# Kernel tuning notes

Measured on AMD Instinct MI355X. Metric: run time of the kernel, lower is better.

## Reference

```python
import jax, jax.numpy as jnp
import numpy as np

NUM_HEADS = 8


def setup_inputs() -> dict:
    key = jax.random.key(0)
    ks = jax.random.split(key, 7)
    R, C, E = 64, 2048, 512
    x = jax.random.normal(ks[0], (R, C, E), dtype=jnp.float32)
    s = 0.02
    Wq = jax.random.normal(ks[1], (E, E), dtype=jnp.float32) * s
    bq = jax.random.normal(ks[2], (E,), dtype=jnp.float32) * s
    Wk = jax.random.normal(ks[3], (E, E), dtype=jnp.float32) * s
    bk = jax.random.normal(ks[4], (E,), dtype=jnp.float32) * s
    Wv = jax.random.normal(ks[5], (E, E), dtype=jnp.float32) * s
    bv = jax.random.normal(ks[6], (E,), dtype=jnp.float32) * s
    return {"x": x, "Wq": Wq, "bq": bq, "Wk": Wk, "bk": bk, "Wv": Wv, "bv": bv}


def reference(x, Wq, bq, Wk, bk, Wv, bv):
    # pred() path (forward default return_attn=True)
    R, C, E = x.shape
    H = NUM_HEADS
    D = E // H
    # projections (torch Linear: x @ W.T + b), split heads -> [R, H, C, D]
    q = (x @ Wq.T + bq).reshape(R, C, H, D).transpose(0, 2, 1, 3)
    k = (x @ Wk.T + bk).reshape(R, C, H, D).transpose(0, 2, 1, 3)
    v = (x @ Wv.T + bv).reshape(R, C, H, D).transpose(0, 2, 1, 3)
    # mean over rows for q, k -> [H, C, D]; v keeps rows -> [R, H, C, D]
    q = q.mean(axis=0)
    k = k.mean(axis=0)
    # kernelized attention: softmax over feature dim for q, over seq dim for k
    q = jax.nn.softmax(q, axis=-1) * (D ** -0.5)
    k = jax.nn.softmax(k, axis=-2)
    # explicit attention map [H, C, C] (pred path materializes it)
    attn_weights = jnp.einsum('hnd,hmd->hnm', q, k)
    # linear-attention: kv outer-sum context then q @ context
    context = jnp.einsum('hnd,bhne->bhde', k, v)        # [R, H, D, D]
    out = jnp.einsum('hnd,bhde->bhne', q, context)      # [R, H, C, D]
    out = out.transpose(0, 2, 1, 3).reshape(R, C, E)
    return out, attn_weights
```

## Files before the change

### kernel.cpp

```cpp
#include <hip/hip_runtime.h>

#define R_ 64
#define C_ 2048
#define E_ 512
#define H_ 8
#define D_ 64

constexpr int CE = C_ * E_;
constexpr long long OUT_ELEMS = 67108864LL;

typedef __attribute__((ext_vector_type(8))) short bf16x8;
typedef __attribute__((ext_vector_type(4))) float f32x4;

__device__ __forceinline__ unsigned short f2bf(float f) {
    union { float f; unsigned u; } v; v.f = f;
    unsigned r = v.u + 0x7FFFu + ((v.u >> 16) & 1u);
    return (unsigned short)(r >> 16);
}

typedef __attribute__((address_space(1))) unsigned char glob_t;
typedef __attribute__((address_space(3))) unsigned char lds_t;
__device__ __forceinline__ void gld_lds16(const unsigned short* g, unsigned short* l) {
    __builtin_amdgcn_global_load_lds((const glob_t*)g, (lds_t*)l, 16, 0, 0);
}

__global__ __launch_bounds__(256) void prep(const float* __restrict__ x,
                                            float* __restrict__ xbar,
                                            unsigned short* __restrict__ xT) {
    __shared__ float Ts[64][65];
    int c0 = blockIdx.x * 64, e0 = blockIdx.y * 64;
    int t = threadIdx.x;
    int r = t >> 2;
    int cs = (t & 3) * 16;
    float acc[16] = {};
    for (int b = 0; b < 64; ++b) {
        const float* xp = x + ((size_t)b * C_ + c0 + r) * E_ + e0 + cs;
        float vv[16];
        float4 v0 = *(const float4*)(xp);
        float4 v1 = *(const float4*)(xp + 4);
        float4 v2 = *(const float4*)(xp + 8);
        float4 v3 = *(const float4*)(xp + 12);
        vv[0]=v0.x; vv[1]=v0.y; vv[2]=v0.z; vv[3]=v0.w;
        vv[4]=v1.x; vv[5]=v1.y; vv[6]=v1.z; vv[7]=v1.w;
        vv[8]=v2.x; vv[9]=v2.y; vv[10]=v2.z; vv[11]=v2.w;
        vv[12]=v3.x; vv[13]=v3.y; vv[14]=v3.z; vv[15]=v3.w;
        #pragma unroll
        for (int i = 0; i < 16; ++i) acc[i] += vv[i];
        __syncthreads();
        #pragma unroll
        for (int i = 0; i < 16; ++i) Ts[cs + i][r] = vv[i];
        __syncthreads();
        unsigned short ob[16];
        #pragma unroll
        for (int i = 0; i < 16; ++i) ob[i] = f2bf(Ts[r][cs + i]);
        unsigned short* op = xT + ((size_t)b * E_ + e0 + r) * C_ + c0 + cs;
        *(bf16x8*)(op)     = *(bf16x8*)(ob);
        *(bf16x8*)(op + 8) = *(bf16x8*)(ob + 8);
    }
    float* xb = xbar + (size_t)(c0 + r) * E_ + e0 + cs;
    #pragma unroll
    for (int i = 0; i < 16; ++i) xb[i] = acc[i] * 0.015625f;
}

__global__ __launch_bounds__(256) void gemm_nt(const float* __restrict__ A, int lda,
                                               const float* __restrict__ B, int ldb,
                                               float* __restrict__ Cmat, int ldc, int K,
                                               const float* __restrict__ bias, int biasPerM) {
    __shared__ float As[64][65];
    __shared__ float Bs[64][65];
    int m0 = blockIdx.y * 64, n0 = blockIdx.x * 64;
    int t = threadIdx.x, tx = t & 15, ty = t >> 4;
    float acc[4][4] = {};
    for (int k0 = 0; k0 < K; k0 += 64) {
        #pragma unroll
        for (int i = 0; i < 4; ++i) {
            int rr = ty + i * 16, cc = tx * 4;
            float4 av = *(const float4*)(A + (size_t)(m0 + rr) * lda + k0 + cc);
            As[rr][cc] = av.x; As[rr][cc + 1] = av.y; As[rr][cc + 2] = av.z; As[rr][cc + 3] = av.w;
            float4 bv = *(const float4*)(B + (size_t)(n0 + rr) * ldb + k0 + cc);
            Bs[cc][rr] = bv.x; Bs[cc + 1][rr] = bv.y; Bs[cc + 2][rr] = bv.z; Bs[cc + 3][rr] = bv.w;
        }
        __syncthreads();
        for (int kk = 0; kk < 64; ++kk) {
            float a[4];
            #pragma unroll
            for (int i = 0; i < 4; ++i) a[i] = As[ty + 16 * i][kk];
            float4 b4 = *(const float4*)(&Bs[kk][tx * 4]);
            #pragma unroll
            for (int i = 0; i < 4; ++i) {
                acc[i][0] += a[i] * b4.x; acc[i][1] += a[i] * b4.y;
                acc[i][2] += a[i] * b4.z; acc[i][3] += a[i] * b4.w;
            }
        }
        __syncthreads();
    }
    #pragma unroll
    for (int i = 0; i < 4; ++i) {
        int m = m0 + ty + 16 * i, n = n0 + tx * 4;
        float4 o;
        if (biasPerM) {
            float bm = bias[m];
            o.x = acc[i][0] + bm; o.y = acc[i][1] + bm; o.z = acc[i][2] + bm; o.w = acc[i][3] + bm;
        } else {
            o.x = acc[i][0] + bias[n]; o.y = acc[i][1] + bias[n + 1];
            o.z = acc[i][2] + bias[n + 2]; o.w = acc[i][3] + bias[n + 3];
        }
        *(float4*)(Cmat + (size_t)m * ldc + n) = o;
    }
}

__global__ __launch_bounds__(256) void softmax_q(float* __restrict__ q) {
    int t = threadIdx.x;
    int chunk = blockIdx.x * 4 + (t >> 6);
    int lane = t & 63;
    float* p = q + (size_t)chunk * 64;
    float v = p[lane];
    float m = v;
    for (int o = 32; o; o >>= 1) m = fmaxf(m, __shfl_xor(m, o));
    float e = expf(v - m);
    float s = e;
    for (int o = 32; o; o >>= 1) s += __shfl_xor(s, o);
    p[lane] = e / s * 0.125f;
}

__global__ __launch_bounds__(256) void softmax_k(float* __restrict__ kT,
                                                 unsigned short* __restrict__ kbf) {
    __shared__ float red[256];
    int j = blockIdx.x, t = threadIdx.x;
    float* row = kT + (size_t)j * C_;
    float vals[8];
    float mx = -1e30f;
    #pragma unroll
    for (int i = 0; i < 8; ++i) { vals[i] = row[t + 256 * i]; mx = fmaxf(mx, vals[i]); }
    red[t] = mx; __syncthreads();
    for (int s = 128; s; s >>= 1) { if (t < s) red[t] = fmaxf(red[t], red[t + s]); __syncthreads(); }
    mx = red[0]; __syncthreads();
    float sum = 0.f;
    #pragma unroll
    for (int i = 0; i < 8; ++i) { vals[i] = expf(vals[i] - mx); sum += vals[i]; }
    red[t] = sum; __syncthreads();
    for (int s = 128; s; s >>= 1) { if (t < s) red[t] += red[t + s]; __syncthreads(); }
    float inv = 1.0f / red[0];
    #pragma unroll
    for (int i = 0; i < 8; ++i) {
        float v = vals[i] * inv;
        row[t + 256 * i] = v;
        kbf[(size_t)j * C_ + t + 256 * i] = f2bf(v);
    }
}

__global__ __launch_bounds__(256) void t_gemm(const unsigned short* __restrict__ Abf,
                                              const unsigned short* __restrict__ xT,
                                              float* __restrict__ Tout) {
    __shared__ __align__(16) unsigned short As[128 * 32];
    __shared__ __align__(16) unsigned short Bs[128 * 32];
    const int b = blockIdx.z;
    const unsigned short* Bg = xT + (size_t)b * CE;
    const int m0 = blockIdx.y * 128, n0 = blockIdx.x * 128;
    const int t = threadIdx.x, lane = t & 63, w = t >> 6;
    const int wm = (w >> 1) * 64, wn = (w & 1) * 64;
    const int l15 = lane & 15, quad = lane >> 4;
    const int srow = t >> 2, sseg = (t & 3) * 8;

    f32x4 acc[4][4];
    #pragma unroll
    for (int i = 0; i < 4; ++i)
        #pragma unroll
        for (int j = 0; j < 4; ++j) acc[i][j] = (f32x4){0.f, 0.f, 0.f, 0.f};

    for (int k0 = 0; k0 < C_; k0 += 32) {
        gld_lds16(Abf + (size_t)(m0 + srow) * C_ + k0 + sseg,        &As[srow * 32 + sseg]);
        gld_lds16(Abf + (size_t)(m0 + 64 + srow) * C_ + k0 + sseg,   &As[(64 + srow) * 32 + sseg]);
        gld_lds16(Bg  + (size_t)(n0 + srow) * C_ + k0 + sseg,        &Bs[srow * 32 + sseg]);
        gld_lds16(Bg  + (size_t)(n0 + 64 + srow) * C_ + k0 + sseg,   &Bs[(64 + srow) * 32 + sseg]);
        __syncthreads();
        bf16x8 af[4], bfr[4];
        #pragma unroll
        for (int mi = 0; mi < 4; ++mi)
            af[mi] = *(const bf16x8*)(&As[(wm + mi * 16 + l15) * 32 + quad * 8]);
        #pragma unroll
        for (int ni = 0; ni < 4; ++ni)
            bfr[ni] = *(const bf16x8*)(&Bs[(wn + ni * 16 + l15) * 32 + quad * 8]);
        #pragma unroll
        for (int mi = 0; mi < 4; ++mi)
            #pragma unroll
            for (int ni = 0; ni < 4; ++ni)
                acc[mi][ni] = __builtin_amdgcn_mfma_f32_16x16x32_bf16(
                    af[mi], bfr[ni], acc[mi][ni], 0, 0, 0);
        __syncthreads();
    }
    float* To = Tout + (size_t)b * 262144;
    #pragma unroll
    for (int mi = 0; mi < 4; ++mi)
        #pragma unroll
        for (int ni = 0; ni < 4; ++ni)
            #pragma unroll
            for (int r = 0; r < 4; ++r) {
                int m = m0 + wm + mi * 16 + quad * 4 + r;
                int n = n0 + wn + ni * 16 + l15;
                To[(size_t)m * 512 + n] = acc[mi][ni][r];
            }
}

__global__ __launch_bounds__(256) void ctx_kernel(const float* __restrict__ T,
                                                  const float* __restrict__ Wv,
                                                  const float* __restrict__ bv,
                                                  float* __restrict__ ctx) {
    __shared__ float As[64][65];
    __shared__ float Bs[64][65];
    int z = blockIdx.x, b = z >> 3, h = z & 7;
    const float* A = T + (size_t)b * 262144 + (size_t)h * 64 * 512;
    const float* B = Wv + (size_t)h * 64 * 512;
    int t = threadIdx.x, tx = t & 15, ty = t >> 4;
    float acc[4][4] = {};
    for (int k0 = 0; k0 < 512; k0 += 64) {
        #pragma unroll
        for (int i = 0; i < 4; ++i) {
            int rr = ty + i * 16, cc = tx * 4;
            float4 av = *(const float4*)(A + (size_t)rr * 512 + k0 + cc);
            As[rr][cc] = av.x; As[rr][cc + 1] = av.y; As[rr][cc + 2] = av.z; As[rr][cc + 3] = av.w;
            float4 bvv = *(const float4*)(B + (size_t)rr * 512 + k0 + cc);
            Bs[cc][rr] = bvv.x; Bs[cc + 1][rr] = bvv.y; Bs[cc + 2][rr] = bvv.z; Bs[cc + 3][rr] = bvv.w;
        }
        __syncthreads();
        for (int kk = 0; kk < 64; ++kk) {
            float a[4];
            #pragma unroll
            for (int i = 0; i < 4; ++i) a[i] = As[ty + 16 * i][kk];
            float4 b4 = *(const float4*)(&Bs[kk][tx * 4]);
            #pragma unroll
            for (int i = 0; i < 4; ++i) {
                acc[i][0] += a[i] * b4.x; acc[i][1] += a[i] * b4.y;
                acc[i][2] += a[i] * b4.z; acc[i][3] += a[i] * b4.w;
            }
        }
        __syncthreads();
    }
    #pragma unroll
    for (int i = 0; i < 4; ++i) {
        int d = ty + 16 * i, e = tx * 4;
        float4 o;
        o.x = acc[i][0] + bv[h * 64 + e];     o.y = acc[i][1] + bv[h * 64 + e + 1];
        o.z = acc[i][2] + bv[h * 64 + e + 2]; o.w = acc[i][3] + bv[h * 64 + e + 3];
        *(float4*)(ctx + (size_t)z * 4096 + d * 64 + e) = o;
    }
}

__global__ __launch_bounds__(256) void out_kernel(const float* __restrict__ q,
                                                  const float* __restrict__ ctx,
                                                  float* __restrict__ outp) {
    __shared__ float As[64][65];
    __shared__ float Bs[64][65];
    int z = blockIdx.z, b = z >> 3, h = z & 7;
    int m0 = blockIdx.y * 64;
    int t = threadIdx.x, tx = t & 15, ty = t >> 4;
    #pragma unroll
    for (int i = 0; i < 4; ++i) {
        int rr = ty + i * 16, cc = tx * 4;
        float4 av = *(const float4*)(q + (size_t)(m0 + rr) * 512 + h * 64 + cc);
        As[rr][cc] = av.x; As[rr][cc + 1] = av.y; As[rr][cc + 2] = av.z; As[rr][cc + 3] = av.w;
        float4 bvv = *(const float4*)(ctx + (size_t)z * 4096 + rr * 64 + cc);
        Bs[rr][cc] = bvv.x; Bs[rr][cc + 1] = bvv.y; Bs[rr][cc + 2] = bvv.z; Bs[rr][cc + 3] = bvv.w;
    }
    __syncthreads();
    float acc[4][4] = {};
    for (int kk = 0; kk < 64; ++kk) {
        float a[4];
        #pragma unroll
        for (int i = 0; i < 4; ++i) a[i] = As[ty + 16 * i][kk];
        float4 b4 = *(const float4*)(&Bs[kk][tx * 4]);
        #pragma unroll
        for (int i = 0; i < 4; ++i) {
            acc[i][0] += a[i] * b4.x; acc[i][1] += a[i] * b4.y;
            acc[i][2] += a[i] * b4.z; acc[i][3] += a[i] * b4.w;
        }
    }
    #pragma unroll
    for (int i = 0; i < 4; ++i) {
        int n = m0 + ty + 16 * i, e = tx * 4;
        float4 o; o.x = acc[i][0]; o.y = acc[i][1]; o.z = acc[i][2]; o.w = acc[i][3];
        *(float4*)(outp + ((size_t)b * C_ + n) * E_ + h * 64 + e) = o;
    }
}

__global__ __launch_bounds__(256) void attn_kernel(const float* __restrict__ q,
                                                   const float* __restrict__ kT,
                                                   float* __restrict__ attn) {
    __shared__ float As[64][65];
    __shared__ float Bs[64][65];
    int h = blockIdx.z;
    int n0 = blockIdx.y * 64, m0 = blockIdx.x * 64;
    int t = threadIdx.x, tx = t & 15, ty = t >> 4;
    #pragma unroll
    for (int i = 0; i < 4; ++i) {
        int rr = ty + i * 16, cc = tx * 4;
        float4 av = *(const float4*)(q + (size_t)(n0 + rr) * 512 + h * 64 + cc);
        As[rr][cc] = av.x; As[rr][cc + 1] = av.y; As[rr][cc + 2] = av.z; As[rr][cc + 3] = av.w;
        float4 bvv = *(const float4*)(kT + (size_t)(h * 64 + rr) * C_ + m0 + cc);
        Bs[rr][cc] = bvv.x; Bs[rr][cc + 1] = bvv.y; Bs[rr][cc + 2] = bvv.z; Bs[rr][cc + 3] = bvv.w;
    }
    __syncthreads();
    float acc[4][4] = {};
    for (int kk = 0; kk < 64; ++kk) {
        float a[4];
        #pragma unroll
        for (int i = 0; i < 4; ++i) a[i] = As[ty + 16 * i][kk];
        float4 b4 = *(const float4*)(&Bs[kk][tx * 4]);
        #pragma unroll
        for (int i = 0; i < 4; ++i) {
            acc[i][0] += a[i] * b4.x; acc[i][1] += a[i] * b4.y;
            acc[i][2] += a[i] * b4.z; acc[i][3] += a[i] * b4.w;
        }
    }
    #pragma unroll
    for (int i = 0; i < 4; ++i) {
        int n = n0 + ty + 16 * i, m = m0 + tx * 4;
        float4 o; o.x = acc[i][0]; o.y = acc[i][1]; o.z = acc[i][2]; o.w = acc[i][3];
        *(float4*)(attn + (size_t)h * C_ * C_ + (size_t)n * C_ + m) = o;
    }
}

extern "C" void kernel_launch(void* const* d_in, const int* in_sizes, int n_in,
                              void* d_out, int out_size, void* d_ws, size_t ws_size,
                              hipStream_t stream) {
    const float* x  = (const float*)d_in[0];
    const float* Wq = (const float*)d_in[1];
    const float* bq = (const float*)d_in[2];
    const float* Wk = (const float*)d_in[3];
    const float* bk = (const float*)d_in[4];
    const float* Wv = (const float*)d_in[5];
    const float* bv = (const float*)d_in[6];
    float* out = (float*)d_out;

    float* ws = (float*)d_ws;
    float* xbar = ws;
    float* qsm  = ws + 1048576;
    float* kT   = ws + 2097152;
    unsigned short* kbf = (unsigned short*)(ws + 3145728);
    float* ctx  = ws + 3670016;

    unsigned short* xTbf = (unsigned short*)d_out;
    float* Tb = out + OUT_ELEMS;

    prep<<<dim3(32, 8), 256, 0, stream>>>(x, xbar, xTbf);
    gemm_nt<<<dim3(8, 32), 256, 0, stream>>>(xbar, 512, Wq, 512, qsm, 512, 512, bq, 0);
    gemm_nt<<<dim3(32, 8), 256, 0, stream>>>(Wk, 512, xbar, 512, kT, 2048, 512, bk, 1);
    softmax_q<<<4096, 256, 0, stream>>>(qsm);
    softmax_k<<<512, 256, 0, stream>>>(kT, kbf);
    t_gemm<<<dim3(4, 4, 64), 256, 0, stream>>>(kbf, xTbf, Tb);
    ctx_kernel<<<512, 256, 0, stream>>>(Tb, Wv, bv, ctx);
    out_kernel<<<dim3(1, 32, 512), 256, 0, stream>>>(qsm, ctx, out);
    attn_kernel<<<dim3(32, 32, 8), 256, 0, stream>>>(qsm, kT, out + OUT_ELEMS);
}
```

Measured before the change: 1.037 ms.

## Port ctx, output and attention GEMMs to bf16 MFMA with bf16 intermediates

Replaces the fp32 scalar-FMA ctx, out and attn kernels with bf16 MFMA kernels that load fragments straight from global memory. Softmax outputs, the T intermediate and Wv are converted to bf16, and a transposed k copy is written so attn can read contiguous fragments. The bias is folded into the output epilogue, scaled by 0.125, on the basis that the q softmax rows sum to 1. This cuts ALU time and intermediate traffic, at the cost of bf16 precision in the q/k/context path and uncoalesced transposed stores in softmax_k.

```diff
diff --git a/kernel.cpp b/kernel.cpp
--- a/kernel.cpp
+++ b/kernel.cpp
@@ -109,25 +109,27 @@
     }
 }
 
-__global__ __launch_bounds__(256) void softmax_q(float* __restrict__ q) {
+__global__ __launch_bounds__(256) void softmax_q(const float* __restrict__ q,
+                                                 unsigned short* __restrict__ qbf) {
     int t = threadIdx.x;
     int chunk = blockIdx.x * 4 + (t >> 6);
     int lane = t & 63;
-    float* p = q + (size_t)chunk * 64;
+    const float* p = q + (size_t)chunk * 64;
     float v = p[lane];
     float m = v;
     for (int o = 32; o; o >>= 1) m = fmaxf(m, __shfl_xor(m, o));
     float e = expf(v - m);
     float s = e;
     for (int o = 32; o; o >>= 1) s += __shfl_xor(s, o);
-    p[lane] = e / s * 0.125f;
-}
-
-__global__ __launch_bounds__(256) void softmax_k(float* __restrict__ kT,
-                                                 unsigned short* __restrict__ kbf) {
+    qbf[(size_t)chunk * 64 + lane] = f2bf(e / s * 0.125f);
+}
+
+__global__ __launch_bounds__(256) void softmax_k(const float* __restrict__ kT,
+                                                 unsigned short* __restrict__ kbf,
+                                                 unsigned short* __restrict__ kbfT) {
     __shared__ float red[256];
     int j = blockIdx.x, t = threadIdx.x;
-    float* row = kT + (size_t)j * C_;
+    const float* row = kT + (size_t)j * C_;
     float vals[8];
     float mx = -1e30f;
     #pragma unroll
@@ -143,15 +145,25 @@
     float inv = 1.0f / red[0];
     #pragma unroll
     for (int i = 0; i < 8; ++i) {
-        float v = vals[i] * inv;
-        row[t + 256 * i] = v;
-        kbf[(size_t)j * C_ + t + 256 * i] = f2bf(v);
-    }
+        unsigned short bv = f2bf(vals[i] * inv);
+        kbf[(size_t)j * C_ + t + 256 * i] = bv;
+        kbfT[(size_t)(t + 256 * i) * 512 + j] = bv;
+    }
+}
+
+__global__ __launch_bounds__(256) void tobf16(const float* __restrict__ src,
+                                              unsigned short* __restrict__ dst) {
+    int i = blockIdx.x * 256 + threadIdx.x;
+    const float* p = src + (size_t)i * 8;
+    unsigned short o[8];
+    #pragma unroll
+    for (int j = 0; j < 8; ++j) o[j] = f2bf(p[j]);
+    *(bf16x8*)(dst + (size_t)i * 8) = *(bf16x8*)o;
 }
 
 __global__ __launch_bounds__(256) void t_gemm(const unsigned short* __restrict__ Abf,
                                               const unsigned short* __restrict__ xT,
-                                              float* __restrict__ Tout) {
+                                              unsigned short* __restrict__ Tout) {
     __shared__ __align__(16) unsigned short As[128 * 32];
     __shared__ __align__(16) unsigned short Bs[128 * 32];
     const int b = blockIdx.z;
@@ -189,7 +201,7 @@
                     af[mi], bfr[ni], acc[mi][ni], 0, 0, 0);
         __syncthreads();
     }
-    float* To = Tout + (size_t)b * 262144;
+    unsigned short* To = Tout + (size_t)b * 262144;
     #pragma unroll
     for (int mi = 0; mi < 4; ++mi)
         #pragma unroll
@@ -198,126 +210,133 @@
             for (int r = 0; r < 4; ++r) {
                 int m = m0 + wm + mi * 16 + quad * 4 + r;
                 int n = n0 + wn + ni * 16 + l15;
-                To[(size_t)m * 512 + n] = acc[mi][ni][r];
+                To[(size_t)m * 512 + n] = f2bf(acc[mi][ni][r]);
             }
 }
 
-__global__ __launch_bounds__(256) void ctx_kernel(const float* __restrict__ T,
-                                                  const float* __restrict__ Wv,
-                                                  const float* __restrict__ bv,
-                                                  float* __restrict__ ctx) {
-    __shared__ float As[64][65];
-    __shared__ float Bs[64][65];
-    int z = blockIdx.x, b = z >> 3, h = z & 7;
-    const float* A = T + (size_t)b * 262144 + (size_t)h * 64 * 512;
-    const float* B = Wv + (size_t)h * 64 * 512;
-    int t = threadIdx.x, tx = t & 15, ty = t >> 4;
-    float acc[4][4] = {};
-    for (int k0 = 0; k0 < 512; k0 += 64) {
-        #pragma unroll
-        for (int i = 0; i < 4; ++i) {
-            int rr = ty + i * 16, cc = tx * 4;
-            float4 av = *(const float4*)(A + (size_t)rr * 512 + k0 + cc);
-            As[rr][cc] = av.x; As[rr][cc + 1] = av.y; As[rr][cc + 2] = av.z; As[rr][cc + 3] = av.w;
-            float4 bvv = *(const float4*)(B + (size_t)rr * 512 + k0 + cc);
-            Bs[cc][rr] = bvv.x; Bs[cc + 1][rr] = bvv.y; Bs[cc + 2][rr] = bvv.z; Bs[cc + 3][rr] = bvv.w;
-        }
-        __syncthreads();
-        for (int kk = 0; kk < 64; ++kk) {
-            float a[4];
-            #pragma unroll
-            for (int i = 0; i < 4; ++i) a[i] = As[ty + 16 * i][kk];
-            float4 b4 = *(const float4*)(&Bs[kk][tx * 4]);
-            #pragma unroll
-            for (int i = 0; i < 4; ++i) {
-                acc[i][0] += a[i] * b4.x; acc[i][1] += a[i] * b4.y;
-                acc[i][2] += a[i] * b4.z; acc[i][3] += a[i] * b4.w;
+__global__ __launch_bounds__(256) void ctx_mfma(const unsigned short* __restrict__ Tbf,
+                                                const unsigned short* __restrict__ Wvbf,
+                                                unsigned short* __restrict__ ctxT) {
+    const int t = threadIdx.x, lane = t & 63, w = t >> 6;
+    const int z = blockIdx.x * 4 + w, b = z >> 3, h = z & 7;
+    const int l15 = lane & 15, quad = lane >> 4;
+    f32x4 acc[4][4];
+    #pragma unroll
+    for (int i = 0; i < 4; ++i)
+        #pragma unroll
+        for (int j = 0; j < 4; ++j) acc[i][j] = (f32x4){0.f, 0.f, 0.f, 0.f};
+    for (int ks = 0; ks < 16; ++ks) {
+        bf16x8 af[4], bfr[4];
+        #pragma unroll
+        for (int mi = 0; mi < 4; ++mi)
+            af[mi] = *(const bf16x8*)(Wvbf + (size_t)(h * 64 + mi * 16 + l15) * 512 + ks * 32 + quad * 8);
+        #pragma unroll
+        for (int ni = 0; ni < 4; ++ni)
+            bfr[ni] = *(const bf16x8*)(Tbf + ((size_t)b * 512 + h * 64 + ni * 16 + l15) * 512 + ks * 32 + quad * 8);
+        #pragma unroll
+        for (int mi = 0; mi < 4; ++mi)
+            #pragma unroll
+            for (int ni = 0; ni < 4; ++ni)
+                acc[mi][ni] = __builtin_amdgcn_mfma_f32_16x16x32_bf16(
+                    af[mi], bfr[ni], acc[mi][ni], 0, 0, 0);
+    }
+    #pragma unroll
+    for (int mi = 0; mi < 4; ++mi)
+        #pragma unroll
+        for (int ni = 0; ni < 4; ++ni)
+            #pragma unroll
+            for (int r = 0; r < 4; ++r) {
+                int e = mi * 16 + quad * 4 + r, d = ni * 16 + l15;
+                ctxT[(size_t)z * 4096 + e * 64 + d] = f2bf(acc[mi][ni][r]);
             }
-        }
-        __syncthreads();
-    }
-    #pragma unroll
-    for (int i = 0; i < 4; ++i) {
-        int d = ty + 16 * i, e = tx * 4;
-        float4 o;
-        o.x = acc[i][0] + bv[h * 64 + e];     o.y = acc[i][1] + bv[h * 64 + e + 1];
-        o.z = acc[i][2] + bv[h * 64 + e + 2]; o.w = acc[i][3] + bv[h * 64 + e + 3];
-        *(float4*)(ctx + (size_t)z * 4096 + d * 64 + e) = o;
-    }
-}
-
-__global__ __launch_bounds__(256) void out_kernel(const float* __restrict__ q,
-                                                  const float* __restrict__ ctx,
-                                                  float* __restrict__ outp) {
-    __shared__ float As[64][65];
-    __shared__ float Bs[64][65];
-    int z = blockIdx.z, b = z >> 3, h = z & 7;
-    int m0 = blockIdx.y * 64;
-    int t = threadIdx.x, tx = t & 15, ty = t >> 4;
-    #pragma unroll
-    for (int i = 0; i < 4; ++i) {
-        int rr = ty + i * 16, cc = tx * 4;
-        float4 av = *(const float4*)(q + (size_t)(m0 + rr) * 512 + h * 64 + cc);
-        As[rr][cc] = av.x; As[rr][cc + 1] = av.y; As[rr][cc + 2] = av.z; As[rr][cc + 3] = av.w;
-        float4 bvv = *(const float4*)(ctx + (size_t)z * 4096 + rr * 64 + cc);
-        Bs[rr][cc] = bvv.x; Bs[rr][cc + 1] = bvv.y; Bs[rr][cc + 2] = bvv.z; Bs[rr][cc + 3] = bvv.w;
-    }
-    __syncthreads();
-    float acc[4][4] = {};
-    for (int kk = 0; kk < 64; ++kk) {
-        float a[4];
-        #pragma unroll
-        for (int i = 0; i < 4; ++i) a[i] = As[ty + 16 * i][kk];
-        float4 b4 = *(const float4*)(&Bs[kk][tx * 4]);
-        #pragma unroll
-        for (int i = 0; i < 4; ++i) {
-            acc[i][0] += a[i] * b4.x; acc[i][1] += a[i] * b4.y;
-            acc[i][2] += a[i] * b4.z; acc[i][3] += a[i] * b4.w;
-        }
-    }
-    #pragma unroll
-    for (int i = 0; i < 4; ++i) {
-        int n = m0 + ty + 16 * i, e = tx * 4;
-        float4 o; o.x = acc[i][0]; o.y = acc[i][1]; o.z = acc[i][2]; o.w = acc[i][3];
-        *(float4*)(outp + ((size_t)b * C_ + n) * E_ + h * 64 + e) = o;
-    }
-}
-
-__global__ __launch_bounds__(256) void attn_kernel(const float* __restrict__ q,
-                                                   const float* __restrict__ kT,
-                                                   float* __restrict__ attn) {
-    __shared__ float As[64][65];
-    __shared__ float Bs[64][65];
-    int h = blockIdx.z;
-    int n0 = blockIdx.y * 64, m0 = blockIdx.x * 64;
-    int t = threadIdx.x, tx = t & 15, ty = t >> 4;
-    #pragma unroll
-    for (int i = 0; i < 4; ++i) {
-        int rr = ty + i * 16, cc = tx * 4;
-        float4 av = *(const float4*)(q + (size_t)(n0 + rr) * 512 + h * 64 + cc);
-        As[rr][cc] = av.x; As[rr][cc + 1] = av.y; As[rr][cc + 2] = av.z; As[rr][cc + 3] = av.w;
-        float4 bvv = *(const float4*)(kT + (size_t)(h * 64 + rr) * C_ + m0 + cc);
-        Bs[rr][cc] = bvv.x; Bs[rr][cc + 1] = bvv.y; Bs[rr][cc + 2] = bvv.z; Bs[rr][cc + 3] = bvv.w;
-    }
-    __syncthreads();
-    float acc[4][4] = {};
-    for (int kk = 0; kk < 64; ++kk) {
-        float a[4];
-        #pragma unroll
-        for (int i = 0; i < 4; ++i) a[i] = As[ty + 16 * i][kk];
-        float4 b4 = *(const float4*)(&Bs[kk][tx * 4]);
-        #pragma unroll
-        for (int i = 0; i < 4; ++i) {
-            acc[i][0] += a[i] * b4.x; acc[i][1] += a[i] * b4.y;
-            acc[i][2] += a[i] * b4.z; acc[i][3] += a[i] * b4.w;
-        }
-    }
-    #pragma unroll
-    for (int i = 0; i < 4; ++i) {
-        int n = n0 + ty + 16 * i, m = m0 + tx * 4;
-        float4 o; o.x = acc[i][0]; o.y = acc[i][1]; o.z = acc[i][2]; o.w = acc[i][3];
-        *(float4*)(attn + (size_t)h * C_ * C_ + (size_t)n * C_ + m) = o;
-    }
+}
+
+__global__ __launch_bounds__(256) void out_mfma(const unsigned short* __restrict__ qbf,
+                                                const unsigned short* __restrict__ ctxT,
+                                                const float* __restrict__ bv,
+                                                float* __restrict__ outp) {
+    const int b = blockIdx.y;
+    const int n0 = blockIdx.x * 128;
+    const int t = threadIdx.x, lane = t & 63, w = t >> 6;
+    const int wm = (w & 1) * 64;
+    const int h0 = (w >> 1) * 4;
+    const int l15 = lane & 15, quad = lane >> 4;
+    for (int hi = 0; hi < 4; ++hi) {
+        const int h = h0 + hi;
+        f32x4 acc[4][4];
+        #pragma unroll
+        for (int i = 0; i < 4; ++i)
+            #pragma unroll
+            for (int j = 0; j < 4; ++j) acc[i][j] = (f32x4){0.f, 0.f, 0.f, 0.f};
+        #pragma unroll
+        for (int ks = 0; ks < 2; ++ks) {
+            bf16x8 af[4], bfr[4];
+            #pragma unroll
+            for (int mi = 0; mi < 4; ++mi)
+                af[mi] = *(const bf16x8*)(qbf + (size_t)(n0 + wm + mi * 16 + l15) * 512 + h * 64 + ks * 32 + quad * 8);
+            #pragma unroll
+            for (int ni = 0; ni < 4; ++ni)
+                bfr[ni] = *(const bf16x8*)(ctxT + (size_t)(b * 8 + h) * 4096 + (ni * 16 + l15) * 64 + ks * 32 + quad * 8);
+            #pragma unroll
+            for (int mi = 0; mi < 4; ++mi)
+                #pragma unroll
+                for (int ni = 0; ni < 4; ++ni)
+                    acc[mi][ni] = __builtin_amdgcn_mfma_f32_16x16x32_bf16(
+                        af[mi], bfr[ni], acc[mi][ni], 0, 0, 0);
+        }
+        #pragma unroll
+        for (int ni = 0; ni < 4; ++ni) {
+            float bvv = 0.125f * bv[h * 64 + ni * 16 + l15];
+            #pragma unroll
+            for (int mi = 0; mi < 4; ++mi)
+                #pragma unroll
+                for (int r = 0; r < 4; ++r) {
+                    int n = n0 + wm + mi * 16 + quad * 4 + r;
+                    outp[((size_t)b * C_ + n) * E_ + h * 64 + ni * 16 + l15] = acc[mi][ni][r] + bvv;
+                }
+        }
+    }
+}
+
+__global__ __launch_bounds__(256) void attn_mfma(const unsigned short* __restrict__ qbf,
+                                                 const unsigned short* __restrict__ kbfT,
+                                                 float* __restrict__ attn) {
+    const int h = blockIdx.z;
+    const int m0 = blockIdx.x * 128, n0 = blockIdx.y * 128;
+    const int t = threadIdx.x, lane = t & 63, w = t >> 6;
+    const int wm = (w >> 1) * 64, wn = (w & 1) * 64;
+    const int l15 = lane & 15, quad = lane >> 4;
+    f32x4 acc[4][4];
+    #pragma unroll
+    for (int i = 0; i < 4; ++i)
+        #pragma unroll
+        for (int j = 0; j < 4; ++j) acc[i][j] = (f32x4){0.f, 0.f, 0.f, 0.f};
+    #pragma unroll
+    for (int ks = 0; ks < 2; ++ks) {
+        bf16x8 af[4], bfr[4];
+        #pragma unroll
+        for (int mi = 0; mi < 4; ++mi)
+            af[mi] = *(const bf16x8*)(qbf + (size_t)(n0 + wm + mi * 16 + l15) * 512 + h * 64 + ks * 32 + quad * 8);
+        #pragma unroll
+        for (int ni = 0; ni < 4; ++ni)
+            bfr[ni] = *(const bf16x8*)(kbfT + (size_t)(m0 + wn + ni * 16 + l15) * 512 + h * 64 + ks * 32 + quad * 8);
+        #pragma unroll
+        for (int mi = 0; mi < 4; ++mi)
+            #pragma unroll
+            for (int ni = 0; ni < 4; ++ni)
+                acc[mi][ni] = __builtin_amdgcn_mfma_f32_16x16x32_bf16(
+                    af[mi], bfr[ni], acc[mi][ni], 0, 0, 0);
+    }
+    #pragma unroll
+    for (int mi = 0; mi < 4; ++mi)
+        #pragma unroll
+        for (int ni = 0; ni < 4; ++ni)
+            #pragma unroll
+            for (int r = 0; r < 4; ++r) {
+                int n = n0 + wm + mi * 16 + quad * 4 + r;
+                int m = m0 + wn + ni * 16 + l15;
+                attn[(size_t)h * C_ * C_ + (size_t)n * C_ + m] = acc[mi][ni][r];
+            }
 }
 
 extern "C" void kernel_launch(void* const* d_in, const int* in_sizes, int n_in,
@@ -336,19 +355,23 @@
     float* xbar = ws;
     float* qsm  = ws + 1048576;
     float* kT   = ws + 2097152;
-    unsigned short* kbf = (unsigned short*)(ws + 3145728);
-    float* ctx  = ws + 3670016;
+    unsigned short* kbf  = (unsigned short*)(ws + 3145728);
+    unsigned short* kbfT = (unsigned short*)(ws + 3670016);
+    unsigned short* qbf  = (unsigned short*)(ws + 4194304);
+    unsigned short* Wvbf = (unsigned short*)(ws + 4718592);
+    unsigned short* ctxT = (unsigned short*)kT;
 
     unsigned short* xTbf = (unsigned short*)d_out;
-    float* Tb = out + OUT_ELEMS;
+    unsigned short* Tbf  = (unsigned short*)(out + OUT_ELEMS);
 
     prep<<<dim3(32, 8), 256, 0, stream>>>(x, xbar, xTbf);
+    tobf16<<<128, 256, 0, stream>>>(Wv, Wvbf);
     gemm_nt<<<dim3(8, 32), 256, 0, stream>>>(xbar, 512, Wq, 512, qsm, 512, 512, bq, 0);
     gemm_nt<<<dim3(32, 8), 256, 0, stream>>>(Wk, 512, xbar, 512, kT, 2048, 512, bk, 1);
-    softmax_q<<<4096, 256, 0, stream>>>(qsm);
-    softmax_k<<<512, 256, 0, stream>>>(kT, kbf);
-    t_gemm<<<dim3(4, 4, 64), 256, 0, stream>>>(kbf, xTbf, Tb);
-    ctx_kernel<<<512, 256, 0, stream>>>(Tb, Wv, bv, ctx);
-    out_kernel<<<dim3(1, 32, 512), 256, 0, stream>>>(qsm, ctx, out);
-    attn_kernel<<<dim3(32, 32, 8), 256, 0, stream>>>(qsm, kT, out + OUT_ELEMS);
-}
+    softmax_q<<<4096, 256, 0, stream>>>(qsm, qbf);
+    softmax_k<<<512, 256, 0, stream>>>(kT, kbf, kbfT);
+    t_gemm<<<dim3(4, 4, 64), 256, 0, stream>>>(kbf, xTbf, Tbf);
+    ctx_mfma<<<128, 256, 0, stream>>>(Tbf, Wvbf, ctxT);
+    out_mfma<<<dim3(16, 64), 256, 0, stream>>>(qbf, ctxT, bv, out);
+    attn_mfma<<<dim3(16, 16, 8), 256, 0, stream>>>(qbf, kbfT, out + OUT_ELEMS);
+}
```

Measured after the change: 847.8 us. 18.3% less time.
